# Performance work log

Hardware: AMD Instinct MI355X
Metric: run time of the kernel (lower is better)

Reference implementation:

```python
import jax, jax.numpy as jnp
import numpy as np

B, L, C, R = 2, 1024, 32, 16
A_SCALE = 0.05  # keep spectral radius of random 16x16 matrices < 1 for a stable 1024-step recurrence


def setup_inputs() -> dict:
    key = jax.random.key(0)
    k1, k2, k3, k4 = jax.random.split(key, 4)
    A_r = jax.random.normal(k1, (B, L, C, R, R), jnp.float32) * A_SCALE
    A_i = jax.random.normal(k2, (B, L, C, R, R), jnp.float32) * A_SCALE
    X_r = jax.random.normal(k3, (B, L, C, R), jnp.float32)
    X_i = jax.random.normal(k4, (B, L, C, R), jnp.float32)
    return {"A_r": A_r, "A_i": A_i, "X_r": X_r, "X_i": X_i}


def reference(A_r, A_i, X_r, X_i):
    # Complex linear recurrence: Y[0] = X[0]; Y[t] = A[t] @ Y[t-1] + X[t]
    # computed via a log-depth associative scan, matching the Triton pscan_kernel.
    A = jax.lax.complex(A_r, A_i)  # [B, L, C, R, R] complex64
    X = jax.lax.complex(X_r, X_i)  # [B, L, C, R]    complex64

    def combine(left, right):
        a_l, x_l = left
        a_r, x_r = right
        # (a_r @ a_l, a_r @ x_l + x_r) -- same as scan_combine_fn
        a_out = jnp.einsum('blcij,blcjk->blcik', a_r, a_l)
        x_out = jnp.einsum('blcij,blcj->blci', a_r, x_l) + x_r
        return (a_out, x_out)

    _, Y = jax.lax.associative_scan(combine, (A, X), axis=1)
    # Return real/imag stacked (matches torch.view_as_real layout): [B, L, C, R, 2]
    return jnp.stack((Y.real, Y.imag), axis=-1)
```

## Files before the change

kernel.cpp:

```cpp
#include <hip/hip_runtime.h>

#define DEVFN static __device__ __forceinline__

constexpr int kLtot = 1024, kC = 32, kB = 2;
constexpr int kG = 64;
constexpr int kCL = kLtot / kG;
constexpr int kNCH = kB * kC;
constexpr int kNCK = kNCH * kG;

constexpr int kSlotB = 2048;
constexpr int kPbufB = 144;
constexpr int kWaveB = 2 * kSlotB + kPbufB;

typedef int v2i __attribute__((ext_vector_type(2)));
typedef __attribute__((ext_vector_type(4))) float f32x4;
typedef __attribute__((ext_vector_type(8))) short s16x8;

union BFrag { unsigned u[4]; s16x8 v; };

DEVFN void gload16(const void* g, void* l) {
  __builtin_amdgcn_global_load_lds((const __attribute__((address_space(1))) void*)g,
                                   (__attribute__((address_space(3))) void*)l, 16, 0, 0);
}

DEVFN float redpair16(float x) {
  return x + __int_as_float(__builtin_amdgcn_ds_swizzle(__float_as_int(x), 0x401F));
}
DEVFN float redpair32(float x) {
#if __has_builtin(__builtin_amdgcn_permlane32_swap)
  v2i r = __builtin_amdgcn_permlane32_swap(__float_as_int(x), __float_as_int(x), false, false);
  return __int_as_float(r.x) + __int_as_float(r.y);
#else
  return x + __shfl_xor(x, 32);
#endif
}
DEVFN float redq(float x) { return redpair32(redpair16(x)); }

DEVFN void splitpk(float x0, float x1, unsigned& h, unsigned& l) {
  unsigned hh, ll;
  asm("v_cvt_pk_bf16_f32 %0, %1, %2" : "=v"(hh) : "v"(x0), "v"(x1));
  const float b0 = __uint_as_float(hh << 16);
  const float b1 = __uint_as_float(hh & 0xffff0000u);
  const float s0 = x0 - b0, s1 = x1 - b1;
  asm("v_cvt_pk_bf16_f32 %0, %1, %2" : "=v"(ll) : "v"(s0), "v"(s1));
  h = hh; l = ll;
}

DEVFN f32x4 mfma16(const unsigned a[4], const unsigned b[4], f32x4 c) {
  BFrag A, B;
  A.u[0] = a[0]; A.u[1] = a[1]; A.u[2] = a[2]; A.u[3] = a[3];
  B.u[0] = b[0]; B.u[1] = b[1]; B.u[2] = b[2]; B.u[3] = b[3];
  return __builtin_amdgcn_mfma_f32_16x16x32_bf16(A.v, B.v, c, 0, 0, 0);
}

#define PUTW(w, r0_, r1_, i0_, i1_)                                \
  do {                                                             \
    unsigned rh_, rl_, ih_, il_;                                   \
    splitpk((r0_), (r1_), rh_, rl_);                               \
    splitpk((i0_), (i1_), ih_, il_);                               \
    b1h[w] = loQ ? rh_ : (ih_ ^ 0x80008000u);                      \
    b1l[w] = loQ ? rl_ : (il_ ^ 0x80008000u);                      \
    b2h[w] = loQ ? ih_ : rh_;                                      \
    b2l[w] = loQ ? il_ : rl_;                                      \
  } while (0)

__global__ __launch_bounds__(256, 4) void pscan_phase1(
    const float* __restrict__ Ar, const float* __restrict__ Ai,
    const float* __restrict__ Xr, const float* __restrict__ Xi,
    float* __restrict__ Pg, float* __restrict__ Vg) {
  __shared__ __align__(16) float ldsF[4 * (kWaveB / 4)];
  const int lane = threadIdx.x & 63;
  const int wid = threadIdx.x >> 6;
  const int q = lane >> 4, j = lane & 15, h = q & 1;
  const bool loQ = (q < 2);
  const int kq = q, ka = (lane >> 2) & 3, kc = lane & 3;
  const int jv = 4 * kc + ka;

  const int ck = blockIdx.x * 4 + wid;
  const int chain = ck >> 6, g = ck & 63;
  const int bb = chain >> 5, cc = chain & 31;
  const int t0 = g * kCL;

  char* ldsW = (char*)ldsF + wid * kWaveB;
  char* pbase = ldsW + 2 * kSlotB;
  const int aOff = (q >> 1) * 1024 + j * 64 + h * 32;
  const int laneAv = ka * 64 + kq * 16 + kc * 256;

  const size_t aBase = ((size_t)(bb * kLtot + t0) * kC + cc) * 256;
  const size_t xBase2 = ((size_t)(bb * kLtot + t0) * kC + cc) * 16;
  const float* arPtr = Ar + aBase + (size_t)lane * 4;
  const float* aiPtr = Ai + aBase + (size_t)lane * 4;
  const float* xrPtr = Xr + xBase2 + jv;
  const float* xiPtr = Xi + xBase2 + jv;

  char* vwA = pbase + jv * 8;
  const char* vrA = pbase + kq * 32;

  float xrP[2], xiP[2];
  auto issueStep = [&](int t) {
    const size_t ao = (size_t)t * (kC * 256);
    char* sd = ldsW + (t & 1) * kSlotB;
    gload16(arPtr + ao, sd);
    gload16(aiPtr + ao, sd + 1024);
    xrP[t & 1] = xrPtr[(size_t)t * (kC * 16)];
    xiP[t & 1] = xiPtr[(size_t)t * (kC * 16)];
  };

  issueStep(0);
  asm volatile("" ::: "memory");
  issueStep(1);
  asm volatile("" ::: "memory");

  unsigned b1h[4], b1l[4], b2h[4], b2l[4];
  f32x4 accR, accI;
  float vre[4], vim[4], vnr = 0.f, vni = 0.f;

  asm volatile("s_waitcnt vmcnt(4)" ::: "memory");
  {
    const char* s0 = ldsW;
    float R[8], I[8];
#pragma unroll
    for (int e = 0; e < 8; ++e) {
      R[e] = *(const float*)(s0 + (8 * h + e) * 64 + j * 4);
      I[e] = *(const float*)(s0 + 1024 + (8 * h + e) * 64 + j * 4);
    }
    PUTW(0, R[0], R[1], I[0], I[1]);
    PUTW(1, R[2], R[3], I[2], I[3]);
    PUTW(2, R[4], R[5], I[4], I[5]);
    PUTW(3, R[6], R[7], I[6], I[7]);
    const float* xr0 = Xr + xBase2;
    const float* xi0 = Xi + xBase2;
#pragma unroll
    for (int kk = 0; kk < 4; ++kk) {
      vre[kk] = xr0[4 * kq + kk];
      vim[kk] = xi0[4 * kq + kk];
    }
  }
  asm volatile("s_waitcnt lgkmcnt(0)" ::: "memory");
  issueStep(2);
  asm volatile("" ::: "memory");

  auto stepCompute = [&](int t) {
    const char* sb = ldsW + (t & 1) * kSlotB;
    const float4 a0 = *(const float4*)(sb + aOff);
    const float4 a1 = *(const float4*)(sb + aOff + 16);
    unsigned Ah[4], Al[4];
    splitpk(a0.x, a0.y, Ah[0], Al[0]);
    splitpk(a0.z, a0.w, Ah[1], Al[1]);
    splitpk(a1.x, a1.y, Ah[2], Al[2]);
    splitpk(a1.z, a1.w, Ah[3], Al[3]);
    const f32x4 zz = {0.f, 0.f, 0.f, 0.f};
    accR = mfma16(Al, b1h, zz);
    accI = mfma16(Al, b2h, zz);
    accR = mfma16(Ah, b1l, accR);
    accI = mfma16(Ah, b2l, accI);
    accR = mfma16(Ah, b1h, accR);
    accI = mfma16(Ah, b2h, accI);
    {
      const float4 a4 = *(const float4*)(sb + laneAv);
      const float4 b4 = *(const float4*)(sb + laneAv + 1024);
      float pr = a4.x * vre[0] - b4.x * vim[0];
      float pi = a4.x * vim[0] + b4.x * vre[0];
      pr += a4.y * vre[1] - b4.y * vim[1];  pi += a4.y * vim[1] + b4.y * vre[1];
      pr += a4.z * vre[2] - b4.z * vim[2];  pi += a4.z * vim[2] + b4.z * vre[2];
      pr += a4.w * vre[3] - b4.w * vim[3];  pi += a4.w * vim[3] + b4.w * vre[3];
      pr = redq(pr); pi = redq(pi);
      vnr = pr + xrP[t & 1];
      vni = pi + xiP[t & 1];
      if (kq == 0) *(float2*)vwA = make_float2(vnr, vni);
      const float4 v0 = *(const float4*)(vrA);
      const float4 v1 = *(const float4*)(vrA + 16);
      vre[0] = v0.x; vim[0] = v0.y; vre[1] = v0.z; vim[1] = v0.w;
      vre[2] = v1.x; vim[2] = v1.y; vre[3] = v1.z; vim[3] = v1.w;
    }
  };

  auto repack = [&]() {
    const int srcA = j | ((2 * h) << 4);
    const int srcB = srcA + 16;
    PUTW(0, __shfl(accR[0], srcA), __shfl(accR[1], srcA), __shfl(accI[0], srcA), __shfl(accI[1], srcA));
    PUTW(1, __shfl(accR[2], srcA), __shfl(accR[3], srcA), __shfl(accI[2], srcA), __shfl(accI[3], srcA));
    PUTW(2, __shfl(accR[0], srcB), __shfl(accR[1], srcB), __shfl(accI[0], srcB), __shfl(accI[1], srcB));
    PUTW(3, __shfl(accR[2], srcB), __shfl(accR[3], srcB), __shfl(accI[2], srcB), __shfl(accI[3], srcB));
  };

#pragma unroll 2
  for (int t = 1; t < kCL - 2; ++t) {
    asm volatile("s_waitcnt vmcnt(4)" ::: "memory");
    stepCompute(t);
    repack();
    issueStep(t + 2);
  }
  asm volatile("s_waitcnt vmcnt(4)" ::: "memory");
  stepCompute(kCL - 2);
  repack();
  asm volatile("s_waitcnt vmcnt(0)" ::: "memory");
  stepCompute(kCL - 1);

  {
    float* pd = Pg + (size_t)ck * 512;
#pragma unroll
    for (int r = 0; r < 4; ++r) {
      *(float2*)(pd + (4 * q + r) * 32 + j * 2) = make_float2(accR[r], accI[r]);
    }
  }
  if (kq == 0) *(float2*)(Vg + (size_t)ck * 32 + jv * 2) = make_float2(vnr, vni);
}

constexpr int kD2 = 4;
__global__ __launch_bounds__(64, 1) void pscan_phase2(
    const float* __restrict__ Pg, const float* __restrict__ Vg, float* __restrict__ Sg) {
  const int lane = threadIdx.x;
  const int kq = lane >> 4, i = lane & 15;
  const int chain = blockIdx.x;

  const float* pB = Pg + (size_t)chain * kG * 512 + (size_t)i * 32 + 8 * kq;
  const float* vB = Vg + (size_t)chain * kG * 32 + 2 * i;
  float* sB = Sg + (size_t)chain * kG * 32 + 2 * i;

  float4 bP0[kD2], bP1[kD2]; float2 bV[kD2];
#pragma unroll
  for (int d = 0; d < kD2; ++d) {
    bP0[d] = *(const float4*)(pB + (size_t)d * 512);
    bP1[d] = *(const float4*)(pB + (size_t)d * 512 + 4);
    bV[d] = *(const float2*)(vB + (size_t)d * 32);
  }

  float ykr[4] = {0, 0, 0, 0}, yki[4] = {0, 0, 0, 0};
  float ynr = 0.f, yni = 0.f;

  for (int gg = 0; gg < kG; gg += kD2) {
#pragma unroll
    for (int d = 0; d < kD2; ++d) {
      if (kq == 0) *(float2*)(sB + (size_t)(gg + d) * 32) = make_float2(ynr, yni);
      const float4 p0 = bP0[d], p1 = bP1[d];
      const float2 vv = bV[d];
      const int gn = gg + d + kD2;
      if (gn < kG) {
        bP0[d] = *(const float4*)(pB + (size_t)gn * 512);
        bP1[d] = *(const float4*)(pB + (size_t)gn * 512 + 4);
        bV[d] = *(const float2*)(vB + (size_t)gn * 32);
      }
      float tr = p0.x * ykr[0] - p0.y * yki[0] + p0.z * ykr[1] - p0.w * yki[1]
               + p1.x * ykr[2] - p1.y * yki[2] + p1.z * ykr[3] - p1.w * yki[3];
      float ti = p0.x * yki[0] + p0.y * ykr[0] + p0.z * yki[1] + p0.w * ykr[1]
               + p1.x * yki[2] + p1.y * ykr[2] + p1.z * yki[3] + p1.w * ykr[3];
      tr = redq(tr); ti = redq(ti);
      ynr = tr + vv.x;
      yni = ti + vv.y;
#pragma unroll
      for (int kk = 0; kk < 4; ++kk) {
        const int src = (lane & 48) | (4 * kq + kk);
        ykr[kk] = __shfl(ynr, src);
        yki[kk] = __shfl(yni, src);
      }
    }
  }
}

__global__ __launch_bounds__(256, 4) void pscan_phase3(
    const float* __restrict__ Ar, const float* __restrict__ Ai,
    const float* __restrict__ Xr, const float* __restrict__ Xi,
    const float* __restrict__ Sg, float* __restrict__ out) {
  const int lane = threadIdx.x & 63;
  const int wid = threadIdx.x >> 6;
  const int kq = lane >> 4, i = lane & 15;
  const int ck = blockIdx.x * 4 + wid;
  const int chain = ck >> 6, g = ck & 63;
  const int bb = chain >> 5, cc = chain & 31;
  const int t0 = g * kCL;

  const size_t aBase = ((size_t)(bb * kLtot + t0) * kC + cc) * 256 + (size_t)i * 16 + 4 * kq;
  const size_t xBase = ((size_t)(bb * kLtot + t0) * kC + cc) * 16 + i;
  const size_t aStep = (size_t)kC * 256, xStep = (size_t)kC * 16;
  float* outB = out + ((size_t)(bb * kLtot + t0) * kC + cc) * 32 + 2 * i;

  float ynr, yni, ykr[4], yki[4];
  {
    const float2 s = *(const float2*)(Sg + (size_t)ck * 32 + 2 * i);
    ynr = s.x; yni = s.y;
  }
#pragma unroll
  for (int kk = 0; kk < 4; ++kk) {
    const int src = (lane & 48) | (4 * kq + kk);
    ykr[kk] = __shfl(ynr, src);
    yki[kk] = __shfl(yni, src);
  }

  float4 aR[2], aI[2]; float2 xx[2];
  auto loadT = [&](int t, int s) {
    aR[s] = *(const float4*)(Ar + aBase + (size_t)t * aStep);
    aI[s] = *(const float4*)(Ai + aBase + (size_t)t * aStep);
    xx[s].x = Xr[xBase + (size_t)t * xStep];
    xx[s].y = Xi[xBase + (size_t)t * xStep];
  };
  loadT(0, 0);
  loadT(1, 1);

  for (int t = 0; t < kCL; ++t) {
    const int s = t & 1;
    const float4 a4 = aR[s], b4 = aI[s];
    const float2 xv = xx[s];
    float tr = a4.x * ykr[0] - b4.x * yki[0] + a4.y * ykr[1] - b4.y * yki[1]
             + a4.z * ykr[2] - b4.z * yki[2] + a4.w * ykr[3] - b4.w * yki[3];
    float ti = a4.x * yki[0] + b4.x * ykr[0] + a4.y * yki[1] + b4.y * ykr[1]
             + a4.z * yki[2] + b4.z * ykr[2] + a4.w * yki[3] + b4.w * ykr[3];
    tr = redq(tr); ti = redq(ti);
    ynr = tr + xv.x;
    yni = ti + xv.y;
    if (kq == 0) *(float2*)(outB + (size_t)t * (kC * 32)) = make_float2(ynr, yni);
    const int tn = t + 2;
    if (tn < kCL) loadT(tn, s);
#pragma unroll
    for (int kk = 0; kk < 4; ++kk) {
      const int src = (lane & 48) | (4 * kq + kk);
      ykr[kk] = __shfl(ynr, src);
      yki[kk] = __shfl(yni, src);
    }
  }
}

extern "C" void kernel_launch(void* const* d_in, const int* in_sizes, int n_in,
                              void* d_out, int out_size, void* d_ws, size_t ws_size,
                              hipStream_t stream) {
  const float* Ar = (const float*)d_in[0];
  const float* Ai = (const float*)d_in[1];
  const float* Xr = (const float*)d_in[2];
  const float* Xi = (const float*)d_in[3];
  float* Pg = (float*)d_ws;
  float* Vg = Pg + (size_t)kNCK * 512;
  float* Sg = Vg + (size_t)kNCK * 32;

  pscan_phase1<<<kNCK / 4, 256, 0, stream>>>(Ar, Ai, Xr, Xi, Pg, Vg);
  pscan_phase2<<<kNCH, 64, 0, stream>>>(Pg, Vg, Sg);
  pscan_phase3<<<kNCK / 4, 256, 0, stream>>>(Ar, Ai, Xr, Xi, Sg, (float*)d_out);
}
```

Before: 78.11 us.

## Deepen phase1 LDS prefetch ring to three slots and hoist A split ahead

```diff
diff --git a/kernel.cpp b/kernel.cpp
--- a/kernel.cpp
+++ b/kernel.cpp
@@ -8,9 +8,9 @@
 constexpr int kNCH = kB * kC;
 constexpr int kNCK = kNCH * kG;
 
+constexpr int kRing = 3;
 constexpr int kSlotB = 2048;
-constexpr int kPbufB = 144;
-constexpr int kWaveB = 2 * kSlotB + kPbufB;
+constexpr int kWaveB = kRing * kSlotB + 144;
 
 typedef int v2i __attribute__((ext_vector_type(2)));
 typedef __attribute__((ext_vector_type(4))) float f32x4;
@@ -82,12 +82,13 @@
   const int t0 = g * kCL;
 
   char* ldsW = (char*)ldsF + wid * kWaveB;
-  char* pbase = ldsW + 2 * kSlotB;
+  char* pbase = ldsW + kRing * kSlotB;
   const int aOff = (q >> 1) * 1024 + j * 64 + h * 32;
   const int laneAv = ka * 64 + kq * 16 + kc * 256;
 
   const size_t aBase = ((size_t)(bb * kLtot + t0) * kC + cc) * 256;
   const size_t xBase2 = ((size_t)(bb * kLtot + t0) * kC + cc) * 16;
+  const size_t aStep = (size_t)kC * 256, xStep = (size_t)kC * 16;
   const float* arPtr = Ar + aBase + (size_t)lane * 4;
   const float* aiPtr = Ai + aBase + (size_t)lane * 4;
   const float* xrPtr = Xr + xBase2 + jv;
@@ -96,26 +97,28 @@
   char* vwA = pbase + jv * 8;
   const char* vrA = pbase + kq * 32;
 
-  float xrP[2], xiP[2];
+  float xrP[3], xiP[3];
   auto issueStep = [&](int t) {
-    const size_t ao = (size_t)t * (kC * 256);
-    char* sd = ldsW + (t & 1) * kSlotB;
-    gload16(arPtr + ao, sd);
-    gload16(aiPtr + ao, sd + 1024);
-    xrP[t & 1] = xrPtr[(size_t)t * (kC * 16)];
-    xiP[t & 1] = xiPtr[(size_t)t * (kC * 16)];
+    char* sd = ldsW + (t % 3) * kSlotB;
+    gload16(arPtr + (size_t)t * aStep, sd);
+    gload16(aiPtr + (size_t)t * aStep, sd + 1024);
+    xrP[t % 3] = xrPtr[(size_t)t * xStep];
+    xiP[t % 3] = xiPtr[(size_t)t * xStep];
   };
 
   issueStep(0);
   asm volatile("" ::: "memory");
   issueStep(1);
   asm volatile("" ::: "memory");
+  issueStep(2);
+  asm volatile("" ::: "memory");
 
   unsigned b1h[4], b1l[4], b2h[4], b2l[4];
+  unsigned Ah[4], Al[4];
   f32x4 accR, accI;
-  float vre[4], vim[4], vnr = 0.f, vni = 0.f;
-
-  asm volatile("s_waitcnt vmcnt(4)" ::: "memory");
+  float vre[4], vim[4], vnr, vni;
+
+  asm volatile("s_waitcnt vmcnt(8)" ::: "memory");
   {
     const char* s0 = ldsW;
     float R[8], I[8];
@@ -128,27 +131,29 @@
     PUTW(1, R[2], R[3], I[2], I[3]);
     PUTW(2, R[4], R[5], I[4], I[5]);
     PUTW(3, R[6], R[7], I[6], I[7]);
-    const float* xr0 = Xr + xBase2;
-    const float* xi0 = Xi + xBase2;
-#pragma unroll
-    for (int kk = 0; kk < 4; ++kk) {
-      vre[kk] = xr0[4 * kq + kk];
-      vim[kk] = xi0[4 * kq + kk];
-    }
+    vnr = xrP[0]; vni = xiP[0];
+    if (kq == 0) *(float2*)vwA = make_float2(vnr, vni);
+    const float4 v0 = *(const float4*)(vrA);
+    const float4 v1 = *(const float4*)(vrA + 16);
+    vre[0] = v0.x; vim[0] = v0.y; vre[1] = v0.z; vim[1] = v0.w;
+    vre[2] = v1.x; vim[2] = v1.y; vre[3] = v1.z; vim[3] = v1.w;
   }
   asm volatile("s_waitcnt lgkmcnt(0)" ::: "memory");
-  issueStep(2);
-  asm volatile("" ::: "memory");
-
-  auto stepCompute = [&](int t) {
-    const char* sb = ldsW + (t & 1) * kSlotB;
+  issueStep(3);
+  asm volatile("s_waitcnt vmcnt(8)" ::: "memory");
+
+  auto splitA = [&](int sl) {
+    const char* sb = ldsW + sl * kSlotB;
     const float4 a0 = *(const float4*)(sb + aOff);
     const float4 a1 = *(const float4*)(sb + aOff + 16);
-    unsigned Ah[4], Al[4];
     splitpk(a0.x, a0.y, Ah[0], Al[0]);
     splitpk(a0.z, a0.w, Ah[1], Al[1]);
     splitpk(a1.x, a1.y, Ah[2], Al[2]);
     splitpk(a1.z, a1.w, Ah[3], Al[3]);
+  };
+  splitA(1);
+
+  auto stepMFMA = [&](int sl) {
     const f32x4 zz = {0.f, 0.f, 0.f, 0.f};
     accR = mfma16(Al, b1h, zz);
     accI = mfma16(Al, b2h, zz);
@@ -157,6 +162,7 @@
     accR = mfma16(Ah, b1h, accR);
     accI = mfma16(Ah, b2h, accI);
     {
+      const char* sb = ldsW + sl * kSlotB;
       const float4 a4 = *(const float4*)(sb + laneAv);
       const float4 b4 = *(const float4*)(sb + laneAv + 1024);
       float pr = a4.x * vre[0] - b4.x * vim[0];
@@ -165,8 +171,8 @@
       pr += a4.z * vre[2] - b4.z * vim[2];  pi += a4.z * vim[2] + b4.z * vre[2];
       pr += a4.w * vre[3] - b4.w * vim[3];  pi += a4.w * vim[3] + b4.w * vre[3];
       pr = redq(pr); pi = redq(pi);
-      vnr = pr + xrP[t & 1];
-      vni = pi + xiP[t & 1];
+      vnr = pr + xrP[sl];
+      vni = pi + xiP[sl];
       if (kq == 0) *(float2*)vwA = make_float2(vnr, vni);
       const float4 v0 = *(const float4*)(vrA);
       const float4 v1 = *(const float4*)(vrA + 16);
@@ -184,18 +190,23 @@
     PUTW(3, __shfl(accR[2], srcB), __shfl(accR[3], srcB), __shfl(accI[2], srcB), __shfl(accI[3], srcB));
   };
 
-#pragma unroll 2
-  for (int t = 1; t < kCL - 2; ++t) {
-    asm volatile("s_waitcnt vmcnt(4)" ::: "memory");
-    stepCompute(t);
+#pragma unroll 3
+  for (int t = 1; t <= kCL - 4; ++t) {
+    stepMFMA(t % 3);
     repack();
-    issueStep(t + 2);
-  }
+    issueStep(t + 3);
+    asm volatile("s_waitcnt vmcnt(8)" ::: "memory");
+    splitA((t + 1) % 3);
+  }
+  stepMFMA(1);
+  repack();
   asm volatile("s_waitcnt vmcnt(4)" ::: "memory");
-  stepCompute(kCL - 2);
+  splitA(2);
+  stepMFMA(2);
   repack();
   asm volatile("s_waitcnt vmcnt(0)" ::: "memory");
-  stepCompute(kCL - 1);
+  splitA(0);
+  stepMFMA(0);
 
   {
     float* pd = Pg + (size_t)ck * 512;
```

Result: no change. 79.12 us, median of 2 (+1.3%).
